# Kernel tuning notes

Hardware: AMD Instinct MI355X
Metric: run time of the kernel (lower is better)

The kernel has to match this reference:

```python
import jax, jax.numpy as jnp
import numpy as np

SR = 48000
SEG = 960
NH = 8
BASE = 440.0
F0_MIN = 20.0
F0_MAX = 16000.0
EPS = 1e-4
N, C, LF = 16, 256, 200


def _interp_linear(x, Lw):
    # Matches torch F.interpolate(mode='linear', align_corners=False).
    # x: (N, C, Lf) -> (N, C, Lw)
    Lf = x.shape[-1]
    scale = Lf / Lw
    src = (jnp.arange(Lw, dtype=x.dtype) + 0.5) * scale - 0.5
    src = jnp.clip(src, 0.0, Lf - 1)
    i0 = jnp.floor(src).astype(jnp.int32)
    i1 = jnp.minimum(i0 + 1, Lf - 1)
    w = src - i0.astype(x.dtype)
    return x[..., i0] * (1.0 - w) + x[..., i1] * w


def setup_inputs() -> dict:
    key = jax.random.key(0)
    ks = jax.random.split(key, 7)
    scale = 1.0 / np.sqrt(C)
    return {
        "x": jax.random.normal(ks[0], (N, C, LF), dtype=jnp.float32),
        "mag_w": jax.random.uniform(ks[1], (NH, C), jnp.float32, -scale, scale),
        "mag_b": jax.random.uniform(ks[2], (NH,), jnp.float32, -scale, scale),
        "cn_scale": jnp.ones((1, C, 1), jnp.float32),
        "cn_shift": jnp.zeros((1, C, 1), jnp.float32),
        "oct_w": jax.random.uniform(ks[3], (1, C), jnp.float32, -scale, scale),
        "oct_b": jax.random.uniform(ks[4], (1,), jnp.float32, -scale, scale),
    }


def reference(x, mag_w, mag_b, cn_scale, cn_shift, oct_w, oct_b):
    n, c, Lf = x.shape
    Lw = Lf * SEG
    # ChannelNorm (torch.std is unbiased -> ddof=1)
    mu = jnp.mean(x, axis=1, keepdims=True)
    sigma = jnp.std(x, axis=1, keepdims=True, ddof=1) + EPS
    xn = (x - mu) / sigma * cn_scale + cn_shift
    # 1x1 convs
    octave = jnp.einsum('ncl,oc->nol', xn, oct_w) + oct_b[None, :, None]  # (N,1,Lf)
    mag = jnp.exp(jnp.minimum(jnp.einsum('ncl,hc->nhl', x, mag_w) + mag_b[None, :, None], 6.0))  # (N,NH,Lf)
    f0 = jnp.clip(BASE * jnp.exp2(octave), F0_MIN, F0_MAX)  # (N,1,Lf)
    mul = jnp.arange(1, NH + 1, dtype=x.dtype)[None, :, None]
    formants = f0 * mul  # (N,NH,Lf)
    formants_w = _interp_linear(formants, Lw)  # (N,NH,Lw)
    mag_w_up = _interp_linear(mag, Lw)         # (N,NH,Lw)
    t = jnp.cumsum(formants_w / SR, axis=2)
    harmonics = jnp.sin(2.0 * jnp.pi * t) * mag_w_up
    wave = jnp.mean(harmonics, axis=1, keepdims=True)  # (N,1,Lw)
    return wave
```

## Files before the change

kernel.cpp:

```cpp
#include <hip/hip_runtime.h>
#include <math.h>


#define NB   16
#define CCH  256
#define LFR  200
#define LW   192000
#define NHH  8
#define NKM  201
#define CG   8
#define CPB  32
#define INV_SR (1.0 / 48000.0)
#define PSTRIDE 20
#define TPB  4

__device__ inline double wave_sum64(double v) {
    #pragma unroll
    for (int off = 32; off > 0; off >>= 1) v += __shfl_xor(v, off);
    return v;
}
__device__ inline double wave_incl_scan64(double v) {
    int lane = threadIdx.x & 63;
    #pragma unroll
    for (int off = 1; off < 64; off <<= 1) {
        double t = __shfl_up(v, off);
        if (lane >= off) v += t;
    }
    return v;
}

__global__ __launch_bounds__(256)
void hg_partial(const float* __restrict__ x,
                const float* __restrict__ mag_w,
                const float* __restrict__ cn_scale,
                const float* __restrict__ oct_w,
                double* __restrict__ ps, double* __restrict__ ps2,
                double* __restrict__ pdx, float* __restrict__ pmg) {
    int n = blockIdx.x, cg = blockIdx.y;
    int t = threadIdx.x;
    const float* xb = x + (size_t)n * CCH * LFR;
    int cbase = cg * CPB;

    double s = 0.0, s2 = 0.0, dx = 0.0;
    float zm[NHH] = {0.f, 0.f, 0.f, 0.f, 0.f, 0.f, 0.f, 0.f};
    #pragma unroll 8
    for (int cc = 0; cc < CPB; cc++) {
        int c = cbase + cc;
        float xf = (t < LFR) ? xb[(size_t)c * LFR + t] : 0.f;
        double xd = (double)xf;
        double w2 = (double)cn_scale[c] * (double)oct_w[c];
        s += xd;
        s2 = fma(xd, xd, s2);
        dx = fma(xd, w2, dx);
        #pragma unroll
        for (int h = 0; h < NHH; h++)
            zm[h] = fmaf(xf, mag_w[h * CCH + c], zm[h]);
    }
    size_t pi = ((size_t)n * CG + cg) * 256 + t;
    ps[pi] = s; ps2[pi] = s2; pdx[pi] = dx;
    #pragma unroll
    for (int h = 0; h < NHH; h++)
        pmg[(((size_t)n * CG + cg) * NHH + h) * 256 + t] = zm[h];
}

__global__ __launch_bounds__(256)
void hg_tables(const double* __restrict__ ps, const double* __restrict__ ps2,
               const double* __restrict__ pdx, const float* __restrict__ pmg,
               const float* __restrict__ mag_b,
               const float* __restrict__ cn_scale, const float* __restrict__ cn_shift,
               const float* __restrict__ oct_w, const float* __restrict__ oct_b,
               float* __restrict__ params) {
    __shared__ double Fl[LFR];
    __shared__ double Tl[LFR];
    __shared__ float  Mgl[LFR][NHH];
    __shared__ double SAB[2];

    int n = blockIdx.x, tid = threadIdx.x;

    if (tid < 64) {
        double sa = 0.0, sb = 0.0;
        #pragma unroll
        for (int k = 0; k < 4; k++) {
            int c = tid + 64 * k;
            double ow = (double)oct_w[c];
            sa = fma((double)cn_scale[c], ow, sa);
            sb = fma((double)cn_shift[c], ow, sb);
        }
        sa = wave_sum64(sa);
        sb = wave_sum64(sb);
        if (tid == 0) { SAB[0] = sa; SAB[1] = sb; }
    }
    __syncthreads();

    if (tid < LFR) {
        double s = 0.0, s2 = 0.0, dx = 0.0;
        #pragma unroll
        for (int cg = 0; cg < CG; cg++) {
            size_t pi = ((size_t)n * CG + cg) * 256 + tid;
            s += ps[pi]; s2 += ps2[pi]; dx += pdx[pi];
        }
        double mu  = s * (1.0 / 256.0);
        double var = (s2 - s * mu) * (1.0 / 255.0);
        double inv = 1.0 / (sqrt(var) + 1e-4);
        double oct = inv * (dx - mu * SAB[0]) + SAB[1] + (double)oct_b[0];
        double f0  = 440.0 * exp2(oct);
        Fl[tid] = fmin(fmax(f0, 20.0), 16000.0);
        #pragma unroll
        for (int h = 0; h < NHH; h++) {
            float z = 0.f;
            #pragma unroll
            for (int cg = 0; cg < CG; cg++)
                z += pmg[(((size_t)n * CG + cg) * NHH + h) * 256 + tid];
            Mgl[tid][h] = expf(fminf(z + mag_b[h], 6.f));
        }
    }
    __syncthreads();

    if (tid < 64) {
        double carry = 480.0 * Fl[0];
        for (int base = 0; base < LFR; base += 64) {
            int k = base + tid;
            double d = (k < LFR - 1) ? 480.0 * (Fl[k] + Fl[k + 1]) : 0.0;
            double scn = wave_incl_scan64(d);
            if (k < LFR) Tl[k] = carry + scn - d;
            carry += __shfl(scn, 63);
        }
    }
    __syncthreads();

    if (tid < NKM) {
        int km = tid;
        int kc = min(max(km - 1, 0), LFR - 1);
        bool body = (km >= 1 && km <= LFR - 1);
        double Sd = Fl[kc] * INV_SR;
        double Qd = body ? (Fl[km] - Fl[km - 1]) * (INV_SR / 1920.0) : 0.0;
        double Pd = (km == 0) ? (-480.0 * Fl[0] * INV_SR) : Tl[km - 1] * INV_SR;
        double Pp = Pd + 480.0 * Sd + 230400.0 * Qd;
        double Sp = Sd + 960.0 * Qd;
        float* pr = params + ((size_t)n * NKM + km) * PSTRIDE;
        pr[0] = (float)(Pp - floor(Pp));
        pr[1] = (float)Sp;
        pr[2] = (float)Qd;
        pr[3] = 0.f;
        #pragma unroll
        for (int h = 0; h < NHH; h++) {
            float a = Mgl[kc][h];
            pr[4 + h]  = a;
            pr[12 + h] = body ? (Mgl[km][h] - a) : 0.f;
        }
    }
}

__global__ __launch_bounds__(256)
void hg_wave(const float* __restrict__ params, float* __restrict__ out) {
    int tid = threadIdx.x;
    #pragma unroll
    for (int i = 0; i < TPB; i++) {
        int tile = blockIdx.x * TPB + i;
        int n = tile / NKM, km = tile - n * NKM;
        const float4* pb = (const float4*)(params + (size_t)tile * PSTRIDE);
        float4 v0 = pb[0], v1 = pb[1], v2 = pb[2], v3 = pb[3], v4 = pb[4];
        float Pf = v0.x, Sf = v0.y, Qf = v0.z;
        float ma[NHH] = {v1.x, v1.y, v1.z, v1.w, v2.x, v2.y, v2.z, v2.w};
        float md[NHH] = {v3.x, v3.y, v3.z, v3.w, v4.x, v4.y, v4.z, v4.w};

        if (tid >= 240) continue;
        int j0 = 960 * km - 480 + tid * 4;
        if (j0 < 0 || j0 >= LW) continue;

        float r[4];
        #pragma unroll
        for (int u = 0; u < 4; u++) {
            float pc = (float)(tid * 4 - 479 + u);
            float tb = fmaf(pc, fmaf(Qf, pc, Sf), Pf);
            float fr, s1, c1;
            asm("v_fract_f32 %0, %1" : "=v"(fr) : "v"(tb));
            asm("v_sin_f32 %0, %1" : "=v"(s1) : "v"(fr));
            asm("v_cos_f32 %0, %1" : "=v"(c1) : "v"(fr));
            float twoc = c1 + c1;
            float w = (pc + 479.5f) * (1.0f / 960.0f);
            float sp = 0.f, sc = s1;
            float acc = 0.f;
            #pragma unroll
            for (int h = 0; h < NHH; h++) {
                acc = fmaf(fmaf(md[h], w, ma[h]), sc, acc);
                float sn = fmaf(twoc, sc, -sp);
                sp = sc; sc = sn;
            }
            r[u] = acc * 0.125f;
        }
        *(float4*)(out + (size_t)n * LW + j0) = make_float4(r[0], r[1], r[2], r[3]);
    }
}

extern "C" void kernel_launch(void* const* d_in, const int* in_sizes, int n_in,
                              void* d_out, int out_size, void* d_ws, size_t ws_size,
                              hipStream_t stream) {
    const float* x        = (const float*)d_in[0];
    const float* mag_w    = (const float*)d_in[1];
    const float* mag_b    = (const float*)d_in[2];
    const float* cn_scale = (const float*)d_in[3];
    const float* cn_shift = (const float*)d_in[4];
    const float* oct_w    = (const float*)d_in[5];
    const float* oct_b    = (const float*)d_in[6];
    float* out = (float*)d_out;

    double* ps  = (double*)d_ws;
    double* ps2 = ps  + (size_t)NB * CG * 256;
    double* pdx = ps2 + (size_t)NB * CG * 256;
    float*  pmg = (float*)(pdx + (size_t)NB * CG * 256);
    float*  params = pmg + (size_t)NB * CG * NHH * 256;

    hg_partial<<<dim3(NB, CG), dim3(256), 0, stream>>>(
        x, mag_w, cn_scale, oct_w, ps, ps2, pdx, pmg);
    hg_tables<<<dim3(NB), dim3(256), 0, stream>>>(
        ps, ps2, pdx, pmg, mag_b, cn_scale, cn_shift, oct_w, oct_b, params);
    hg_wave<<<dim3((NKM * NB) / TPB), dim3(256), 0, stream>>>(params, out);
}
```

Baseline: 22.79 us.

## Fuse table construction into wave kernel, recomputing tables per block

Merges the per-batch tables kernel into the waveform kernel so each wave block rebuilds f0, phase scan and magnitude tables in shared memory, then synthesizes its four frames directly. This removes one kernel launch and the params buffer round trip through global memory. In exchange every block redundantly reduces the partial sums and runs the serial scan, which adds L2 traffic and latency per block. The 1/8 mean scale is folded into the magnitudes.

Measured after the change: 24.49 us. 1.07x slower.

```diff
diff --git a/kernel.cpp b/kernel.cpp
--- a/kernel.cpp
+++ b/kernel.cpp
@@ -11,8 +11,8 @@
 #define CG   8
 #define CPB  32
 #define INV_SR (1.0 / 48000.0)
-#define PSTRIDE 20
 #define TPB  4
+#define KMB  ((NKM + TPB - 1) / TPB)
 
 __device__ inline double wave_sum64(double v) {
     #pragma unroll
@@ -64,18 +64,19 @@
 }
 
 __global__ __launch_bounds__(256)
-void hg_tables(const double* __restrict__ ps, const double* __restrict__ ps2,
-               const double* __restrict__ pdx, const float* __restrict__ pmg,
-               const float* __restrict__ mag_b,
-               const float* __restrict__ cn_scale, const float* __restrict__ cn_shift,
-               const float* __restrict__ oct_w, const float* __restrict__ oct_b,
-               float* __restrict__ params) {
+void hg_wave(const double* __restrict__ ps, const double* __restrict__ ps2,
+             const double* __restrict__ pdx, const float* __restrict__ pmg,
+             const float* __restrict__ mag_b,
+             const float* __restrict__ cn_scale, const float* __restrict__ cn_shift,
+             const float* __restrict__ oct_w, const float* __restrict__ oct_b,
+             float* __restrict__ out) {
     __shared__ double Fl[LFR];
     __shared__ double Tl[LFR];
     __shared__ float  Mgl[LFR][NHH];
     __shared__ double SAB[2];
 
-    int n = blockIdx.x, tid = threadIdx.x;
+    int n = blockIdx.y;
+    int tid = threadIdx.x;
 
     if (tid < 64) {
         double sa = 0.0, sb = 0.0;
@@ -93,25 +94,25 @@
     __syncthreads();
 
     if (tid < LFR) {
-        double s = 0.0, s2 = 0.0, dx = 0.0;
-        #pragma unroll
-        for (int cg = 0; cg < CG; cg++) {
-            size_t pi = ((size_t)n * CG + cg) * 256 + tid;
-            s += ps[pi]; s2 += ps2[pi]; dx += pdx[pi];
-        }
-        double mu  = s * (1.0 / 256.0);
-        double var = (s2 - s * mu) * (1.0 / 255.0);
+        double s_ = 0.0, s2_ = 0.0, dx_ = 0.0;
+        #pragma unroll
+        for (int cg2 = 0; cg2 < CG; cg2++) {
+            size_t pj = ((size_t)n * CG + cg2) * 256 + tid;
+            s_ += ps[pj]; s2_ += ps2[pj]; dx_ += pdx[pj];
+        }
+        double mu  = s_ * (1.0 / 256.0);
+        double var = (s2_ - s_ * mu) * (1.0 / 255.0);
         double inv = 1.0 / (sqrt(var) + 1e-4);
-        double oct = inv * (dx - mu * SAB[0]) + SAB[1] + (double)oct_b[0];
+        double oct = inv * (dx_ - mu * SAB[0]) + SAB[1] + (double)oct_b[0];
         double f0  = 440.0 * exp2(oct);
         Fl[tid] = fmin(fmax(f0, 20.0), 16000.0);
         #pragma unroll
         for (int h = 0; h < NHH; h++) {
             float z = 0.f;
             #pragma unroll
-            for (int cg = 0; cg < CG; cg++)
-                z += pmg[(((size_t)n * CG + cg) * NHH + h) * 256 + tid];
-            Mgl[tid][h] = expf(fminf(z + mag_b[h], 6.f));
+            for (int cg2 = 0; cg2 < CG; cg2++)
+                z += pmg[(((size_t)n * CG + cg2) * NHH + h) * 256 + tid];
+            Mgl[tid][h] = 0.125f * expf(fminf(z + mag_b[h], 6.f));
         }
     }
     __syncthreads();
@@ -128,8 +129,10 @@
     }
     __syncthreads();
 
-    if (tid < NKM) {
-        int km = tid;
+    #pragma unroll
+    for (int i = 0; i < TPB; i++) {
+        int km = blockIdx.x * TPB + i;
+        if (km >= NKM) break;
         int kc = min(max(km - 1, 0), LFR - 1);
         bool body = (km >= 1 && km <= LFR - 1);
         double Sd = Fl[kc] * INV_SR;
@@ -137,59 +140,45 @@
         double Pd = (km == 0) ? (-480.0 * Fl[0] * INV_SR) : Tl[km - 1] * INV_SR;
         double Pp = Pd + 480.0 * Sd + 230400.0 * Qd;
         double Sp = Sd + 960.0 * Qd;
-        float* pr = params + ((size_t)n * NKM + km) * PSTRIDE;
-        pr[0] = (float)(Pp - floor(Pp));
-        pr[1] = (float)Sp;
-        pr[2] = (float)Qd;
-        pr[3] = 0.f;
+        float Pf = (float)(Pp - floor(Pp));
+        float Sf = (float)Sp;
+        float Qf = (float)Qd;
+        float ma[NHH], md[NHH];
         #pragma unroll
         for (int h = 0; h < NHH; h++) {
             float a = Mgl[kc][h];
-            pr[4 + h]  = a;
-            pr[12 + h] = body ? (Mgl[km][h] - a) : 0.f;
-        }
-    }
-}
-
-__global__ __launch_bounds__(256)
-void hg_wave(const float* __restrict__ params, float* __restrict__ out) {
-    int tid = threadIdx.x;
-    #pragma unroll
-    for (int i = 0; i < TPB; i++) {
-        int tile = blockIdx.x * TPB + i;
-        int n = tile / NKM, km = tile - n * NKM;
-        const float4* pb = (const float4*)(params + (size_t)tile * PSTRIDE);
-        float4 v0 = pb[0], v1 = pb[1], v2 = pb[2], v3 = pb[3], v4 = pb[4];
-        float Pf = v0.x, Sf = v0.y, Qf = v0.z;
-        float ma[NHH] = {v1.x, v1.y, v1.z, v1.w, v2.x, v2.y, v2.z, v2.w};
-        float md[NHH] = {v3.x, v3.y, v3.z, v3.w, v4.x, v4.y, v4.z, v4.w};
-
-        if (tid >= 240) continue;
-        int j0 = 960 * km - 480 + tid * 4;
-        if (j0 < 0 || j0 >= LW) continue;
-
-        float r[4];
-        #pragma unroll
-        for (int u = 0; u < 4; u++) {
-            float pc = (float)(tid * 4 - 479 + u);
-            float tb = fmaf(pc, fmaf(Qf, pc, Sf), Pf);
-            float fr, s1, c1;
-            asm("v_fract_f32 %0, %1" : "=v"(fr) : "v"(tb));
-            asm("v_sin_f32 %0, %1" : "=v"(s1) : "v"(fr));
-            asm("v_cos_f32 %0, %1" : "=v"(c1) : "v"(fr));
-            float twoc = c1 + c1;
-            float w = (pc + 479.5f) * (1.0f / 960.0f);
-            float sp = 0.f, sc = s1;
-            float acc = 0.f;
-            #pragma unroll
-            for (int h = 0; h < NHH; h++) {
-                acc = fmaf(fmaf(md[h], w, ma[h]), sc, acc);
-                float sn = fmaf(twoc, sc, -sp);
-                sp = sc; sc = sn;
+            ma[h] = a;
+            md[h] = body ? (Mgl[km][h] - a) : 0.f;
+        }
+
+        if (tid < 240) {
+            int j0 = 960 * km - 480 + tid * 4;
+            if (j0 >= 0 && j0 < LW) {
+                float r[4];
+                #pragma unroll
+                for (int u = 0; u < 4; u++) {
+                    float pc = (float)(tid * 4 - 479 + u);
+                    float tb = fmaf(pc, fmaf(Qf, pc, Sf), Pf);
+                    float fr, s1, c1;
+                    asm("v_fract_f32 %0, %1" : "=v"(fr) : "v"(tb));
+                    asm("v_sin_f32 %0, %1" : "=v"(s1) : "v"(fr));
+                    asm("v_cos_f32 %0, %1" : "=v"(c1) : "v"(fr));
+                    float twoc = c1 + c1;
+                    float w = (pc + 479.5f) * (1.0f / 960.0f);
+                    float sp = 0.f, sc = s1;
+                    float acc = 0.f;
+                    #pragma unroll
+                    for (int h = 0; h < NHH; h++) {
+                        acc = fmaf(fmaf(md[h], w, ma[h]), sc, acc);
+                        float sn = fmaf(twoc, sc, -sp);
+                        sp = sc; sc = sn;
+                    }
+                    r[u] = acc;
+                }
+                *(float4*)(out + (size_t)n * LW + j0) =
+                    make_float4(r[0], r[1], r[2], r[3]);
             }
-            r[u] = acc * 0.125f;
-        }
-        *(float4*)(out + (size_t)n * LW + j0) = make_float4(r[0], r[1], r[2], r[3]);
+        }
     }
 }
 
@@ -209,11 +198,9 @@
     double* ps2 = ps  + (size_t)NB * CG * 256;
     double* pdx = ps2 + (size_t)NB * CG * 256;
     float*  pmg = (float*)(pdx + (size_t)NB * CG * 256);
-    float*  params = pmg + (size_t)NB * CG * NHH * 256;
 
     hg_partial<<<dim3(NB, CG), dim3(256), 0, stream>>>(
         x, mag_w, cn_scale, oct_w, ps, ps2, pdx, pmg);
-    hg_tables<<<dim3(NB), dim3(256), 0, stream>>>(
-        ps, ps2, pdx, pmg, mag_b, cn_scale, cn_shift, oct_w, oct_b, params);
-    hg_wave<<<dim3((NKM * NB) / TPB), dim3(256), 0, stream>>>(params, out);
-}
+    hg_wave<<<dim3(KMB, NB), dim3(256), 0, stream>>>(
+        ps, ps2, pdx, pmg, mag_b, cn_scale, cn_shift, oct_w, oct_b, out);
+}
```
